# Kernel tuning notes

Measured on AMD Instinct MI355X. Metric: run time of the kernel, lower is better.

## Reference

```python
import jax, jax.numpy as jnp
import numpy as np

B, F, INP, S = 2048, 50, 2, 1024
LN_EPS = 1e-3
UPDATE_BIAS = -1.0
_TRUNC = 0.8796256610342398  # trunc-normal std correction from weight_init


def _std(fan_in, fan_out):
    return np.sqrt(2.0 / (fan_in + fan_out)) / _TRUNC


def setup_inputs() -> dict:
    key = jax.random.key(0)
    k_act, k_emb, k_gru, k_dec = jax.random.split(key, 4)
    return {
        "action": jax.random.normal(k_act, (B, F, INP), dtype=jnp.float32),
        "W_emb": jax.random.normal(k_emb, (INP, S), dtype=jnp.float32) * _std(INP, S),
        "W_gru": jax.random.normal(k_gru, (2 * S, 3 * S), dtype=jnp.float32) * _std(2 * S, 3 * S),
        "ln_gamma": jnp.ones((3 * S,), dtype=jnp.float32),
        "ln_beta": jnp.zeros((3 * S,), dtype=jnp.float32),
        "W_dec": jax.random.normal(k_dec, (S, INP), dtype=jnp.float32) * _std(S, INP),
        "b_dec": jnp.zeros((INP,), dtype=jnp.float32),
    }


def reference(action, W_emb, W_gru, ln_gamma, ln_beta, W_dec, b_dec):
    # action: [b, f, inp]
    emb = jnp.einsum("bfi,is->bfs", action, W_emb)  # [b, f, s]

    def step(prev, x_t):
        # prev, x_t: [b, s]
        parts = jnp.concatenate([x_t, prev], axis=-1) @ W_gru  # [b, 3s]
        mu = parts.mean(-1, keepdims=True)
        var = parts.var(-1, keepdims=True)
        parts = (parts - mu) / jnp.sqrt(var + LN_EPS) * ln_gamma + ln_beta
        reset, cand, update = jnp.split(parts, 3, axis=-1)
        reset = jax.nn.sigmoid(reset)
        cand = jnp.tanh(reset * cand)
        update = jax.nn.sigmoid(update + UPDATE_BIAS)
        h = update * cand + (1.0 - update) * prev
        return h, None

    prev0 = jnp.zeros_like(emb[:, 0])
    h_last, _ = jax.lax.scan(step, prev0, jnp.swapaxes(emb, 0, 1))  # scan over f
    outputs = h_last @ W_dec + b_dec  # [b, inp]
    return h_last[:, None], outputs[:, None]
```

## Files before the change

kernel.cpp:

```cpp
#include <hip/hip_runtime.h>

typedef unsigned short u16;
typedef unsigned int   u32;
typedef _Float16       f16;

#define B_SZ 2048
#define S_SZ 1024
#define N3   3072
#define F_SZ 50

typedef f16    f16x8 __attribute__((ext_vector_type(8)));
typedef f16    f16x4 __attribute__((ext_vector_type(4)));
typedef float  f32x4 __attribute__((ext_vector_type(4)));
typedef u32    u32x4 __attribute__((ext_vector_type(4)));

__device__ __forceinline__ void glds16(const void* g, void* l) {
    __builtin_amdgcn_global_load_lds(
        (const __attribute__((address_space(1))) u32*)g,
        (__attribute__((address_space(3))) u32*)l, 16, 0, 0);
}

__global__ __launch_bounds__(256) void make_mx(
    const float* __restrict__ We, const float* __restrict__ Wg,
    float* __restrict__ Mx)
{
    int j  = blockIdx.x * 256 + threadIdx.x;
    int k0 = blockIdx.y * 64;
    float s0 = 0.f, s1 = 0.f;
    #pragma unroll 4
    for (int k = k0; k < k0 + 64; k++) {
        float w = Wg[(size_t)k * N3 + j];
        s0 += We[k] * w;
        s1 += We[S_SZ + k] * w;
    }
    atomicAdd(&Mx[j], s0);
    atomicAdd(&Mx[N3 + j], s1);
}

__global__ __launch_bounds__(256) void transpose_w(
    const float* __restrict__ Wg, f16* __restrict__ Wt)
{
    __shared__ float tile[32][33];
    int n0 = blockIdx.x * 32, k0 = blockIdx.y * 32;
    int c = threadIdx.x & 31, r = threadIdx.x >> 5;
    #pragma unroll
    for (int s = 0; s < 4; s++) {
        int rr = r + s * 8;
        tile[rr][c] = Wg[(size_t)(S_SZ + k0 + rr) * N3 + n0 + c];
    }
    __syncthreads();
    #pragma unroll
    for (int s = 0; s < 4; s++) {
        int rr = r + s * 8;
        Wt[(size_t)(n0 + rr) * S_SZ + k0 + c] = (f16)tile[c][rr];
    }
}

__global__ __launch_bounds__(256) void gemm_step(
    const f16* __restrict__ Wt,
    const f16* __restrict__ hh,
    const float* __restrict__ Mx,
    const float* __restrict__ act,
    f16* __restrict__ parts,
    int t)
{
    __shared__ __align__(16) f16 As[64 * 64];
    __shared__ __align__(16) f16 Bs[128 * 64];
    const int n0 = blockIdx.x * 128;
    const int m0 = blockIdx.y * 64;
    const int tid  = threadIdx.x;
    const int lane = tid & 63;
    const int wave = tid >> 6;
    const int wr = (wave >> 1) * 32;
    const int wc = (wave & 1) * 64;
    const int quad = lane >> 4, lrow = lane & 15;
    const int swz = (lrow & 7) * 8;

    const int lrow8 = lane >> 3;
    const int scolh = ((lane & 7) * 8) ^ (lrow8 * 8);

    float mx0[4], mx1[4];
    #pragma unroll
    for (int j = 0; j < 4; j++) {
        int n = n0 + wc + j * 16 + lrow;
        mx0[j] = Mx[n]; mx1[j] = Mx[N3 + n];
    }

    f32x4 acc[2][4];
    #pragma unroll
    for (int i = 0; i < 2; i++)
        #pragma unroll
        for (int j = 0; j < 4; j++)
            acc[i][j] = (f32x4){0.f, 0.f, 0.f, 0.f};

    for (int kb = 0; kb < S_SZ; kb += 64) {
        __syncthreads();
        #pragma unroll
        for (int c = 0; c < 2; c++) {
            int ch = wave * 2 + c;
            int row = ch * 8 + lrow8;
            glds16(&hh[(size_t)(m0 + row) * S_SZ + kb + scolh], &As[ch * 512]);
        }
        #pragma unroll
        for (int c = 0; c < 4; c++) {
            int ch = wave * 4 + c;
            int row = ch * 8 + lrow8;
            glds16(&Wt[(size_t)(n0 + row) * S_SZ + kb + scolh], &Bs[ch * 512]);
        }
        __syncthreads();
        #pragma unroll
        for (int kk = 0; kk < 64; kk += 32) {
            f16x8 a[2], b[4];
            #pragma unroll
            for (int i = 0; i < 2; i++)
                a[i] = __builtin_bit_cast(f16x8,
                    *(const u32x4*)&As[(wr + i * 16 + lrow) * 64 +
                                       ((kk + quad * 8) ^ swz)]);
            #pragma unroll
            for (int j = 0; j < 4; j++)
                b[j] = __builtin_bit_cast(f16x8,
                    *(const u32x4*)&Bs[(wc + j * 16 + lrow) * 64 +
                                       ((kk + quad * 8) ^ swz)]);
            #pragma unroll
            for (int i = 0; i < 2; i++)
                #pragma unroll
                for (int j = 0; j < 4; j++)
                    acc[i][j] = __builtin_amdgcn_mfma_f32_16x16x32_f16(
                        a[i], b[j], acc[i][j], 0, 0, 0);
        }
    }

    #pragma unroll
    for (int i = 0; i < 2; i++) {
        #pragma unroll
        for (int rr = 0; rr < 4; rr++) {
            int m = m0 + wr + i * 16 + quad * 4 + rr;
            float a0 = act[((size_t)m * F_SZ + t) * 2 + 0];
            float a1 = act[((size_t)m * F_SZ + t) * 2 + 1];
            #pragma unroll
            for (int j = 0; j < 4; j++) {
                int n = n0 + wc + j * 16 + lrow;
                parts[(size_t)m * N3 + n] =
                    (f16)(acc[i][j][rr] + a0 * mx0[j] + a1 * mx1[j]);
            }
        }
    }
}

__global__ __launch_bounds__(256) void ln_gate_step(
    const f16* __restrict__ parts,
    const float* __restrict__ gamma,
    const float* __restrict__ beta,
    f16* __restrict__ hh,
    float* __restrict__ hout,
    int t)
{
    const int tid = threadIdx.x;
    const int r2  = tid >> 7;
    const int tl  = tid & 127;
    const int row = blockIdx.x * 2 + r2;
    const f16* p = parts + (size_t)row * N3 + tl * 8;

    float v[24];
    float s = 0.f, ss = 0.f;
    #pragma unroll
    for (int g = 0; g < 3; g++) {
        f16x8 x = *(const f16x8*)(p + g * S_SZ);
        #pragma unroll
        for (int e = 0; e < 8; e++) {
            float f = (float)x[e];
            v[g * 8 + e] = f;
            s += f; ss += f * f;
        }
    }
    #pragma unroll
    for (int o = 1; o < 64; o <<= 1) {
        s  += __shfl_xor(s, o);
        ss += __shfl_xor(ss, o);
    }
    __shared__ float red[8];
    int wave = tid >> 6, lane = tid & 63;
    if (lane == 0) { red[wave] = s; red[4 + wave] = ss; }
    __syncthreads();
    float S  = red[r2 * 2] + red[r2 * 2 + 1];
    float SS = red[4 + r2 * 2] + red[4 + r2 * 2 + 1];
    float mean = S * (1.f / N3);
    float var  = SS * (1.f / N3) - mean * mean;
    float rstd = rsqrtf(var + 1e-3f);

    float nv[24];
    #pragma unroll
    for (int g = 0; g < 3; g++) {
        f32x4 g0 = *(const f32x4*)(gamma + g * S_SZ + tl * 8);
        f32x4 g1 = *(const f32x4*)(gamma + g * S_SZ + tl * 8 + 4);
        f32x4 b0 = *(const f32x4*)(beta  + g * S_SZ + tl * 8);
        f32x4 b1 = *(const f32x4*)(beta  + g * S_SZ + tl * 8 + 4);
        #pragma unroll
        for (int e = 0; e < 4; e++) {
            nv[g * 8 + e]     = (v[g * 8 + e]     - mean) * rstd * g0[e] + b0[e];
            nv[g * 8 + e + 4] = (v[g * 8 + e + 4] - mean) * rstd * g1[e] + b1[e];
        }
    }

    size_t hbase = (size_t)row * S_SZ + tl * 8;
    f16x8 hp = *(const f16x8*)(hh + hbase);
    f16x8 hs;
    f32x4 ho0, ho1;
    #pragma unroll
    for (int e = 0; e < 8; e++) {
        float rg = 1.f / (1.f + __expf(-nv[e]));
        float x  = rg * nv[8 + e];
        float tt = __expf(-2.f * fabsf(x));
        float cg = __builtin_copysignf((1.f - tt) / (1.f + tt), x);
        float ug = 1.f / (1.f + __expf(-(nv[16 + e] - 1.f)));
        float hv = ug * cg + (1.f - ug) * (float)hp[e];
        hs[e] = (f16)hv;
        if (e < 4) ho0[e] = hv; else ho1[e - 4] = hv;
    }
    *(f16x8*)(hh + hbase) = hs;
    if (t == F_SZ - 1) {
        *(f32x4*)(hout + hbase)     = ho0;
        *(f32x4*)(hout + hbase + 4) = ho1;
    }
}

__global__ __launch_bounds__(256) void final_out(
    const float* __restrict__ h, const float* __restrict__ Wd,
    const float* __restrict__ bd, float* __restrict__ out)
{
    int row = blockIdx.x * 4 + (threadIdx.x >> 6);
    int lane = threadIdx.x & 63;
    const float* hr = h + (size_t)row * S_SZ;
    float s0 = 0.f, s1 = 0.f;
    #pragma unroll
    for (int k = lane; k < S_SZ; k += 64) {
        float x = hr[k];
        s0 += x * Wd[k * 2];
        s1 += x * Wd[k * 2 + 1];
    }
    #pragma unroll
    for (int o = 32; o > 0; o >>= 1) {
        s0 += __shfl_down(s0, o);
        s1 += __shfl_down(s1, o);
    }
    if (lane == 0) {
        out[(size_t)B_SZ * S_SZ + row * 2 + 0] = s0 + bd[0];
        out[(size_t)B_SZ * S_SZ + row * 2 + 1] = s1 + bd[1];
    }
}

extern "C" void kernel_launch(void* const* d_in, const int* in_sizes, int n_in,
                              void* d_out, int out_size, void* d_ws, size_t ws_size,
                              hipStream_t stream)
{
    const float* act = (const float*)d_in[0];
    const float* We  = (const float*)d_in[1];
    const float* Wg  = (const float*)d_in[2];
    const float* lng = (const float*)d_in[3];
    const float* lnb = (const float*)d_in[4];
    const float* Wd  = (const float*)d_in[5];
    const float* bd  = (const float*)d_in[6];
    float* out = (float*)d_out;

    char* ws = (char*)d_ws;
    f16*   Wt    = (f16*)ws;
    float* Mx    = (float*)(ws + 6291456);
    f16*   hh    = (f16*)(ws + 6316032);
    f16*   parts = (f16*)(ws + 10510336);

    hipMemsetAsync(hh, 0, (size_t)B_SZ * S_SZ * 2, stream);
    hipMemsetAsync(Mx, 0, 2 * N3 * 4, stream);
    make_mx<<<dim3(N3 / 256, 16), 256, 0, stream>>>(We, Wg, Mx);
    transpose_w<<<dim3(N3 / 32, S_SZ / 32), 256, 0, stream>>>(Wg, Wt);

    for (int t = 0; t < F_SZ; t++) {
        gemm_step<<<dim3(24, 32), 256, 0, stream>>>(Wt, hh, Mx, act, parts, t);
        ln_gate_step<<<B_SZ / 2, 256, 0, stream>>>(parts, lng, lnb, hh, out, t);
    }
    final_out<<<B_SZ / 4, 256, 0, stream>>>(out, Wd, bd, out);
}
```

Baseline: 1.548 ms.

## Use 2-wave 64x128 GEMM tiles with LDS-staged coalesced output stores

The per-step GEMM now runs with 128 threads (two waves), and each wave computes a 64x64 sub-tile instead of 32x64. This doubles the MFMA work per wave relative to its LDS fragment loads. The grid is swapped so that blockIdx.x walks the batch dimension, which changes the order blocks are scheduled and how the shared weight columns are reused. The epilogue stages the fp16 results through a padded shared-memory tile, then writes 16-byte coalesced rows instead of scattered 2-byte stores. In exchange, each thread holds more accumulator registers and issues more global-to-LDS loads, which may lower occupancy.

```diff
diff --git a/kernel.cpp b/kernel.cpp
--- a/kernel.cpp
+++ b/kernel.cpp
@@ -56,7 +56,7 @@
     }
 }
 
-__global__ __launch_bounds__(256) void gemm_step(
+__global__ __launch_bounds__(128, 3) void gemm_step(
     const f16* __restrict__ Wt,
     const f16* __restrict__ hh,
     const float* __restrict__ Mx,
@@ -64,17 +64,19 @@
     f16* __restrict__ parts,
     int t)
 {
-    __shared__ __align__(16) f16 As[64 * 64];
-    __shared__ __align__(16) f16 Bs[128 * 64];
-    const int n0 = blockIdx.x * 128;
-    const int m0 = blockIdx.y * 64;
+    __shared__ __align__(16) f16 smem[12288];
+    f16* As = smem;
+    f16* Bs = smem + 4096;
+    f16* Cs = smem;
+
+    const int m0 = blockIdx.x * 64;
+    const int n0 = blockIdx.y * 128;
     const int tid  = threadIdx.x;
     const int lane = tid & 63;
     const int wave = tid >> 6;
-    const int wr = (wave >> 1) * 32;
-    const int wc = (wave & 1) * 64;
+    const int wc   = wave * 64;
     const int quad = lane >> 4, lrow = lane & 15;
-    const int swz = (lrow & 7) * 8;
+    const int swz  = (lrow & 7) * 8;
 
     const int lrow8 = lane >> 3;
     const int scolh = ((lane & 7) * 8) ^ (lrow8 * 8);
@@ -86,35 +88,35 @@
         mx0[j] = Mx[n]; mx1[j] = Mx[N3 + n];
     }
 
-    f32x4 acc[2][4];
-    #pragma unroll
-    for (int i = 0; i < 2; i++)
+    f32x4 acc[4][4];
+    #pragma unroll
+    for (int i = 0; i < 4; i++)
         #pragma unroll
         for (int j = 0; j < 4; j++)
             acc[i][j] = (f32x4){0.f, 0.f, 0.f, 0.f};
 
     for (int kb = 0; kb < S_SZ; kb += 64) {
         __syncthreads();
-        #pragma unroll
-        for (int c = 0; c < 2; c++) {
-            int ch = wave * 2 + c;
-            int row = ch * 8 + lrow8;
-            glds16(&hh[(size_t)(m0 + row) * S_SZ + kb + scolh], &As[ch * 512]);
-        }
         #pragma unroll
         for (int c = 0; c < 4; c++) {
             int ch = wave * 4 + c;
             int row = ch * 8 + lrow8;
+            glds16(&hh[(size_t)(m0 + row) * S_SZ + kb + scolh], &As[ch * 512]);
+        }
+        #pragma unroll
+        for (int c = 0; c < 8; c++) {
+            int ch = wave * 8 + c;
+            int row = ch * 8 + lrow8;
             glds16(&Wt[(size_t)(n0 + row) * S_SZ + kb + scolh], &Bs[ch * 512]);
         }
         __syncthreads();
         #pragma unroll
         for (int kk = 0; kk < 64; kk += 32) {
-            f16x8 a[2], b[4];
-            #pragma unroll
-            for (int i = 0; i < 2; i++)
+            f16x8 a[4], b[4];
+            #pragma unroll
+            for (int i = 0; i < 4; i++)
                 a[i] = __builtin_bit_cast(f16x8,
-                    *(const u32x4*)&As[(wr + i * 16 + lrow) * 64 +
+                    *(const u32x4*)&As[(i * 16 + lrow) * 64 +
                                        ((kk + quad * 8) ^ swz)]);
             #pragma unroll
             for (int j = 0; j < 4; j++)
@@ -122,7 +124,7 @@
                     *(const u32x4*)&Bs[(wc + j * 16 + lrow) * 64 +
                                        ((kk + quad * 8) ^ swz)]);
             #pragma unroll
-            for (int i = 0; i < 2; i++)
+            for (int i = 0; i < 4; i++)
                 #pragma unroll
                 for (int j = 0; j < 4; j++)
                     acc[i][j] = __builtin_amdgcn_mfma_f32_16x16x32_f16(
@@ -130,19 +132,30 @@
         }
     }
 
-    #pragma unroll
-    for (int i = 0; i < 2; i++) {
+    __syncthreads();
+    #pragma unroll
+    for (int i = 0; i < 4; i++) {
         #pragma unroll
         for (int rr = 0; rr < 4; rr++) {
-            int m = m0 + wr + i * 16 + quad * 4 + rr;
+            int mrow = i * 16 + quad * 4 + rr;
+            int m = m0 + mrow;
             float a0 = act[((size_t)m * F_SZ + t) * 2 + 0];
             float a1 = act[((size_t)m * F_SZ + t) * 2 + 1];
             #pragma unroll
-            for (int j = 0; j < 4; j++) {
-                int n = n0 + wc + j * 16 + lrow;
-                parts[(size_t)m * N3 + n] =
+            for (int j = 0; j < 4; j++)
+                Cs[mrow * 132 + wc + j * 16 + lrow] =
                     (f16)(acc[i][j][rr] + a0 * mx0[j] + a1 * mx1[j]);
-            }
+        }
+    }
+    __syncthreads();
+    {
+        const int cseg = (tid & 15) * 8;
+        const int rb   = tid >> 4;
+        #pragma unroll
+        for (int p = 0; p < 8; p++) {
+            int row = p * 8 + rb;
+            *(u32x4*)&parts[(size_t)(m0 + row) * N3 + n0 + cseg] =
+                *(const u32x4*)&Cs[row * 132 + cseg];
         }
     }
 }
@@ -274,7 +287,7 @@
     transpose_w<<<dim3(N3 / 32, S_SZ / 32), 256, 0, stream>>>(Wg, Wt);
 
     for (int t = 0; t < F_SZ; t++) {
-        gemm_step<<<dim3(24, 32), 256, 0, stream>>>(Wt, hh, Mx, act, parts, t);
+        gemm_step<<<dim3(32, 24), 128, 0, stream>>>(Wt, hh, Mx, act, parts, t);
         ln_gate_step<<<B_SZ / 2, 256, 0, stream>>>(parts, lng, lnb, hh, out, t);
     }
     final_out<<<B_SZ / 4, 256, 0, stream>>>(out, Wd, bd, out);
```

New measurement: 1.507 ms. 1.03x faster.
